# Optimization experiments

Measured on AMD Instinct MI355X. Metric: run time of the kernel, lower is better.

The kernel has to match this reference:

```python
import jax, jax.numpy as jnp
import numpy as np

R = 3.9
EPS = 0.3
BETA = 0.15
STEPS = 15
CLAMP = 1e-4


def setup_inputs() -> dict:
    key = jax.random.key(0)
    k1, k2 = jax.random.split(key)
    B, C, H, W = 64, 4, 512, 512
    drive = jax.random.uniform(k1, (B, C, H, W), dtype=jnp.float32)
    # frozen depthwise 3x3 kernel, normalized to sum 1 per channel (matches torch buffer init)
    K_raw = jnp.abs(jax.random.uniform(k2, (C, 1, 3, 3), dtype=jnp.float32))
    K = K_raw / jnp.sum(K_raw, axis=(-1, -2), keepdims=True)
    return {"drive": drive, "K": K}


def _depthwise_conv(x, K):
    # x: [B,C,H,W], K: [C,1,3,3] -> depthwise 3x3 conv, padding=1
    C = x.shape[1]
    return jax.lax.conv_general_dilated(
        x, K, window_strides=(1, 1), padding="SAME",
        dimension_numbers=("NCHW", "OIHW", "NCHW"),
        feature_group_count=C)


def reference(drive, K):
    grid = drive
    for _ in range(STEPS):
        mapped = R * grid * (1.0 - grid)          # logistic map
        local = _depthwise_conv(mapped, K)         # 3x3 depthwise coupling
        physics = (1.0 - EPS) * mapped + EPS * local
        grid = (1.0 - BETA) * physics + BETA * drive
    return jnp.clip(grid, CLAMP, 1.0 - CLAMP)
```

## Files before the change

kernel.cpp:

```cpp
#include <hip/hip_runtime.h>

#define IMG  512
#define TR   48
#define TC   112
#define RH   8
#define RLW  132
#define PR   66

__device__ __forceinline__ float mapf(float g) {
    float t = 3.9f * g;
    return t - t * g;
}

#define RD(P, M) do {                       \
    const float* _p = (P);                  \
    (M)[0] = _p[97 + pj];                   \
    (M)[1] = _p[pj];                        \
    (M)[2] = _p[33 + pj];                   \
    (M)[3] = _p[65 + pj];                   \
    (M)[4] = _p[98 + pj];                   \
    (M)[5] = _p[1 + pj];                    \
} while (0)

__global__ __launch_bounds__(512) void cml_round(
    const float* __restrict__ src,
    const float* __restrict__ drv,
    const float* __restrict__ Kw,
    float* __restrict__ dst,
    int steps, int do_clip)
{
    __shared__ float B[PR * RLW];

    const int tid = threadIdx.x;
    const int bid = blockIdx.x;
    const int bc  = bid / 55;
    const int tl  = bid % 55;
    const int gy0 = (tl / 5) * TR - RH;
    const int gx0 = (tl % 5) * TC - RH;
    const float* __restrict__ simg = src + (size_t)bc * (IMG*IMG);
    const float* __restrict__ dimg = drv + (size_t)bc * (IMG*IMG);
    float*       __restrict__ oimg = dst + (size_t)bc * (IMG*IMG);

    float kk[9];
    {
        const float c2 = 0.85f * 0.3f;
        const float* kp = Kw + (bc & 3) * 9;
#pragma unroll
        for (int q = 0; q < 9; q++) kk[q] = c2 * kp[q];
        kk[4] += 0.85f * 0.7f;
    }

    const int pj  = tid & 31;
    const int pi  = tid >> 5;
    const int y0  = pi * 4;
    const int gxb = gx0 + pj * 4;
    const float fxc = ((unsigned)gxb < IMG) ? 1.0f : 0.0f;

    float dvs[16];
#pragma unroll
    for (int rr = 0; rr < 4; rr++) {
        const int gy = gy0 + y0 + rr;
        float4 dv = make_float4(0.f, 0.f, 0.f, 0.f);
        if ((unsigned)gy < IMG && (unsigned)gxb < IMG)
            dv = *(const float4*)(dimg + gy*IMG + gxb);
        dvs[rr*4+0] = 0.15f * dv.x;
        dvs[rr*4+1] = 0.15f * dv.y;
        dvs[rr*4+2] = 0.15f * dv.z;
        dvs[rr*4+3] = 0.15f * dv.w;
    }

    for (int u = tid; u < PR * 32; u += 512) {
        const int r = u >> 5;
        const int p = u & 31;
        const int gy  = gy0 + r - 1;
        const int gxq = gx0 + p * 4;
        const bool rowok = (unsigned)gy < IMG;
        float4 v = make_float4(0.f, 0.f, 0.f, 0.f);
        if (rowok && (unsigned)gxq < IMG)
            v = *(const float4*)(simg + gy*IMG + gxq);
        float* row = B + r * RLW;
        row[p]      = mapf(v.x);
        row[33 + p] = mapf(v.y);
        row[65 + p] = mapf(v.z);
        row[98 + p] = mapf(v.w);
        if (p == 0) {
            float e = (rowok && (unsigned)(gx0 - 1) < IMG)
                    ? simg[gy*IMG + gx0 - 1] : 0.f;
            row[97] = mapf(e);
        }
        if (p == 31) {
            float e = (rowok && (unsigned)(gx0 + 128) < IMG)
                    ? simg[gy*IMG + gx0 + 128] : 0.f;
            row[32] = mapf(e);
        }
    }
    __syncthreads();

    float st[16];
#pragma unroll 1
    for (int step = 0; step < steps - 1; step++) {
        {
            float a[6], b6[6], c6[6];
            const float* p = B + y0 * RLW;
            RD(p, a);  p += RLW;
            RD(p, b6);
#pragma unroll
            for (int rr = 0; rr < 4; rr++) {
                p += RLW;
                RD(p, c6);
                const float ff = (((unsigned)(gy0 + y0 + rr) < IMG) ? 1.0f : 0.0f) * fxc;
#pragma unroll
                for (int k = 0; k < 4; k++) {
                    float s = dvs[rr*4+k];
                    s += kk[0]*a[k]  + kk[1]*a[k+1]  + kk[2]*a[k+2];
                    s += kk[3]*b6[k] + kk[4]*b6[k+1] + kk[5]*b6[k+2];
                    s += kk[6]*c6[k] + kk[7]*c6[k+1] + kk[8]*c6[k+2];
                    const float t = 3.9f * s;
                    st[rr*4+k] = (t - t*s) * ff;
                }
#pragma unroll
                for (int q = 0; q < 6; q++) { a[q] = b6[q]; b6[q] = c6[q]; }
            }
        }
        __syncthreads();
#pragma unroll
        for (int rr = 0; rr < 4; rr++) {
            float* w = B + (y0 + 1 + rr) * RLW;
            w[pj]      = st[rr*4+0];
            w[33 + pj] = st[rr*4+1];
            w[65 + pj] = st[rr*4+2];
            w[98 + pj] = st[rr*4+3];
        }
        __syncthreads();
    }

    {
        float a[6], b6[6], c6[6];
        const float* p = B + y0 * RLW;
        RD(p, a);  p += RLW;
        RD(p, b6);
#pragma unroll
        for (int rr = 0; rr < 4; rr++) {
            p += RLW;
            RD(p, c6);
#pragma unroll
            for (int k = 0; k < 4; k++) {
                float s = dvs[rr*4+k];
                s += kk[0]*a[k]  + kk[1]*a[k+1]  + kk[2]*a[k+2];
                s += kk[3]*b6[k] + kk[4]*b6[k+1] + kk[5]*b6[k+2];
                s += kk[6]*c6[k] + kk[7]*c6[k+1] + kk[8]*c6[k+2];
                st[rr*4+k] = s;
            }
#pragma unroll
            for (int q = 0; q < 6; q++) { a[q] = b6[q]; b6[q] = c6[q]; }
        }
    }
    if (pi >= 2 && pi <= 13 && pj >= 2 && pj <= 29) {
#pragma unroll
        for (int rr = 0; rr < 4; rr++) {
            const int gy = gy0 + y0 + rr;
            if (gy < IMG && gxb + 3 < IMG) {
                float4 v = make_float4(st[rr*4+0], st[rr*4+1],
                                       st[rr*4+2], st[rr*4+3]);
                if (do_clip) {
                    v.x = fminf(fmaxf(v.x, 1e-4f), 1.0f - 1e-4f);
                    v.y = fminf(fmaxf(v.y, 1e-4f), 1.0f - 1e-4f);
                    v.z = fminf(fmaxf(v.z, 1e-4f), 1.0f - 1e-4f);
                    v.w = fminf(fmaxf(v.w, 1e-4f), 1.0f - 1e-4f);
                }
                *(float4*)(oimg + gy*IMG + gxb) = v;
            }
        }
    }
}

#define TILE  128
#define OFF_Y 16
#define OFF_X 18
#define BUFY  160
#define BUFX  164
#define LW    172
#define NP    1014

__device__ __forceinline__ void read_row6(const float* __restrict__ p, int xw,
                                          float* m) {
    const float4 mid = *(const float4*)(p + xw + 4);
    m[0] = p[xw + 3];
    m[1] = mid.x; m[2] = mid.y; m[3] = mid.z; m[4] = mid.w;
    m[5] = p[xw + 8];
}

__global__ __launch_bounds__(1024, 4) void cml_fused(
    const float* __restrict__ drive,
    const float* __restrict__ Kw,
    float* __restrict__ out)
{
    __shared__ float lds[BUFY * LW];
    const int tid = threadIdx.x;
    const int bid = blockIdx.x;
    const int bc  = bid >> 4;
    const int tl  = bid & 15;
    const int gy0 = (tl >> 2) * TILE - OFF_Y;
    const int gx0 = (tl & 3)  * TILE - OFF_X;
    const float* __restrict__ img  = drive + (size_t)bc * (IMG*IMG);
    float*       __restrict__ oimg = out   + (size_t)bc * (IMG*IMG);
    float kk[9];
    {
        const float c2 = 0.85f * 0.3f;
        const float* kp = Kw + (bc & 3) * 9;
#pragma unroll
        for (int q = 0; q < 9; q++) kk[q] = c2 * kp[q];
        kk[4] += 0.85f * 0.7f;
    }
    const int t2 = tid < NP ? tid : NP - 1;
    const int pi = t2 / 39;
    const int pj = t2 - pi * 39;
    const int y0 = 2 + 6 * pi;
    const int xw = 4 * pj;
    float dvs[24], fx[4], fy[6];
#pragma unroll
    for (int k = 0; k < 4; k++)
        fx[k] = ((unsigned)(gx0 + xw + 4 + k) < IMG) ? 1.0f : 0.0f;
#pragma unroll
    for (int rr = 0; rr < 6; rr++) {
        const int gy = gy0 + y0 + rr;
        fy[rr] = ((unsigned)gy < IMG) ? 1.0f : 0.0f;
#pragma unroll
        for (int k = 0; k < 4; k++) {
            const int gx = gx0 + xw + 4 + k;
            dvs[rr*4+k] = (((unsigned)gy < IMG) && ((unsigned)gx < IMG))
                        ? 0.15f * img[gy*IMG + gx] : 0.0f;
        }
    }
    for (int u = tid; u < BUFY * (LW/2); u += 1024) {
        const int yy = u / (LW/2);
        const int xx = (u - yy * (LW/2)) * 2;
        const int gy = gy0 + yy;
        const int gxb = gx0 + xx;
        float2 v = make_float2(0.f, 0.f);
        if (xx < BUFX && (unsigned)gy < IMG && (unsigned)gxb < IMG)
            v = *(const float2*)(img + gy*IMG + gxb);
        v.x = mapf(v.x); v.y = mapf(v.y);
        *(float2*)(lds + yy*LW + xx) = v;
    }
    __syncthreads();
    float st[24];
#pragma unroll 1
    for (int step = 0; step < 14; step++) {
        {
            float a[6], b[6], c[6];
            const float* p = lds + (y0 - 1) * LW;
            read_row6(p, xw, a);  p += LW;
            read_row6(p, xw, b);
#pragma unroll
            for (int rr = 0; rr < 6; rr++) {
                p += LW;
                read_row6(p, xw, c);
                const float fyr = fy[rr];
#pragma unroll
                for (int k = 0; k < 4; k++) {
                    float s = dvs[rr*4+k];
                    s += kk[0]*a[k] + kk[1]*a[k+1] + kk[2]*a[k+2];
                    s += kk[3]*b[k] + kk[4]*b[k+1] + kk[5]*b[k+2];
                    s += kk[6]*c[k] + kk[7]*c[k+1] + kk[8]*c[k+2];
                    const float t = 3.9f * s;
                    st[rr*4+k] = (t - t*s) * fyr * fx[k];
                }
#pragma unroll
                for (int q = 0; q < 6; q++) { a[q] = b[q]; b[q] = c[q]; }
            }
        }
        __syncthreads();
        {
            float* w = lds + y0 * LW + xw + 4;
#pragma unroll
            for (int rr = 0; rr < 6; rr++) {
                *(float4*)w = make_float4(st[rr*4+0], st[rr*4+1],
                                          st[rr*4+2], st[rr*4+3]);
                w += LW;
            }
        }
        __syncthreads();
    }
    {
        float a[6], b[6], c[6];
        const float* p = lds + (y0 - 1) * LW;
        read_row6(p, xw, a);  p += LW;
        read_row6(p, xw, b);
#pragma unroll
        for (int rr = 0; rr < 6; rr++) {
            p += LW;
            read_row6(p, xw, c);
#pragma unroll
            for (int k = 0; k < 4; k++) {
                float s = dvs[rr*4+k];
                s += kk[0]*a[k] + kk[1]*a[k+1] + kk[2]*a[k+2];
                s += kk[3]*b[k] + kk[4]*b[k+1] + kk[5]*b[k+2];
                s += kk[6]*c[k] + kk[7]*c[k+1] + kk[8]*c[k+2];
                st[rr*4+k] = fminf(fmaxf(s, 1e-4f), 1.0f - 1e-4f);
            }
#pragma unroll
            for (int q = 0; q < 6; q++) { a[q] = b[q]; b[q] = c[q]; }
        }
    }
#pragma unroll
    for (int rr = 0; rr < 6; rr++) {
        const int r = y0 + rr;
        if (r >= OFF_Y && r < OFF_Y + TILE) {
#pragma unroll
            for (int h = 0; h < 2; h++) {
                const int col = xw + 4 + 2*h;
                if (col >= OFF_X && col + 1 < OFF_X + TILE) {
                    *(float2*)(oimg + (size_t)(gy0 + r) * IMG + (gx0 + col)) =
                        make_float2(st[rr*4 + 2*h], st[rr*4 + 2*h + 1]);
                }
            }
        }
    }
}

extern "C" void kernel_launch(void* const* d_in, const int* in_sizes, int n_in,
                              void* d_out, int out_size, void* d_ws, size_t ws_size,
                              hipStream_t stream)
{
    const float* drive = (const float*)d_in[0];
    const float* Kw    = (const float*)d_in[1];
    float* out         = (float*)d_out;
    const size_t need  = (size_t)256 * IMG * IMG * sizeof(float);

    if (ws_size >= need) {
        float* g8 = (float*)d_ws;
        cml_round<<<dim3(14080), dim3(512), 0, stream>>>(drive, drive, Kw, g8, 8, 0);
        cml_round<<<dim3(14080), dim3(512), 0, stream>>>(g8, drive, Kw, out, 7, 1);
    } else {
        cml_fused<<<dim3(4096), dim3(1024), 0, stream>>>(drive, Kw, out);
    }
}
```

Measured before the change: 831.9 us.

## Double-buffer LDS grid and keep each thread's own rows in registers

The single shared tile becomes two ping-pong buffers, so each step needs one barrier instead of two. Each thread now keeps its own 4x4 block of the state in registers across steps and reads only the halo (top and bottom rows, left and right edge columns) from LDS, which cuts LDS read traffic. The cost is twice the LDS per block, which can lower the number of resident blocks per CU. The border rows and columns of the second buffer are never initialised. That is only safe if the halo width covers every step of a round.

```diff
diff --git a/kernel.cpp b/kernel.cpp
--- a/kernel.cpp
+++ b/kernel.cpp
@@ -6,20 +6,18 @@
 #define RH   8
 #define RLW  132
 #define PR   66
+#define BUFSZ (PR * RLW)
 
 __device__ __forceinline__ float mapf(float g) {
     float t = 3.9f * g;
     return t - t * g;
 }
 
-#define RD(P, M) do {                       \
+#define RDROW(P, M) do {                    \
     const float* _p = (P);                  \
-    (M)[0] = _p[97 + pj];                   \
-    (M)[1] = _p[pj];                        \
-    (M)[2] = _p[33 + pj];                   \
-    (M)[3] = _p[65 + pj];                   \
-    (M)[4] = _p[98 + pj];                   \
-    (M)[5] = _p[1 + pj];                    \
+    (M)[0] = _p[97]; (M)[5] = _p[1];        \
+    (M)[1] = _p[0];  (M)[4] = _p[98];       \
+    (M)[2] = _p[33]; (M)[3] = _p[65];       \
 } while (0)
 
 __global__ __launch_bounds__(512) void cml_round(
@@ -29,7 +27,7 @@
     float* __restrict__ dst,
     int steps, int do_clip)
 {
-    __shared__ float B[PR * RLW];
+    __shared__ float Bd[2 * BUFSZ];
 
     const int tid = threadIdx.x;
     const int bid = blockIdx.x;
@@ -56,6 +54,11 @@
     const int gxb = gx0 + pj * 4;
     const float fxc = ((unsigned)gxb < IMG) ? 1.0f : 0.0f;
 
+    float ffr[4];
+#pragma unroll
+    for (int rr = 0; rr < 4; rr++)
+        ffr[rr] = (((unsigned)(gy0 + y0 + rr) < IMG) ? 1.0f : 0.0f) * fxc;
+
     float dvs[16];
 #pragma unroll
     for (int rr = 0; rr < 4; rr++) {
@@ -78,7 +81,7 @@
         float4 v = make_float4(0.f, 0.f, 0.f, 0.f);
         if (rowok && (unsigned)gxq < IMG)
             v = *(const float4*)(simg + gy*IMG + gxq);
-        float* row = B + r * RLW;
+        float* row = Bd + r * RLW;
         row[p]      = mapf(v.x);
         row[33 + p] = mapf(v.y);
         row[65 + p] = mapf(v.z);
@@ -97,62 +100,127 @@
     __syncthreads();
 
     float st[16];
+    {
+        const float* q1 = Bd + (y0 + 1) * RLW + pj;
+        const float* q3 = q1 + 2 * RLW;
+        st[0]  = q1[0];        st[4]  = q1[RLW];
+        st[1]  = q1[33];       st[5]  = q1[33 + RLW];
+        st[2]  = q1[65];       st[6]  = q1[65 + RLW];
+        st[3]  = q1[98];       st[7]  = q1[98 + RLW];
+        st[8]  = q3[0];        st[12] = q3[RLW];
+        st[9]  = q3[33];       st[13] = q3[33 + RLW];
+        st[10] = q3[65];       st[14] = q3[65 + RLW];
+        st[11] = q3[98];       st[15] = q3[98 + RLW];
+    }
+
+    float* cur = Bd;
+    float* nxt = Bd + BUFSZ;
+
 #pragma unroll 1
     for (int step = 0; step < steps - 1; step++) {
-        {
-            float a[6], b6[6], c6[6];
-            const float* p = B + y0 * RLW;
-            RD(p, a);  p += RLW;
-            RD(p, b6);
-#pragma unroll
-            for (int rr = 0; rr < 4; rr++) {
-                p += RLW;
-                RD(p, c6);
-                const float ff = (((unsigned)(gy0 + y0 + rr) < IMG) ? 1.0f : 0.0f) * fxc;
-#pragma unroll
-                for (int k = 0; k < 4; k++) {
-                    float s = dvs[rr*4+k];
-                    s += kk[0]*a[k]  + kk[1]*a[k+1]  + kk[2]*a[k+2];
-                    s += kk[3]*b6[k] + kk[4]*b6[k+1] + kk[5]*b6[k+2];
-                    s += kk[6]*c6[k] + kk[7]*c6[k+1] + kk[8]*c6[k+2];
-                    const float t = 3.9f * s;
-                    st[rr*4+k] = (t - t*s) * ff;
-                }
-#pragma unroll
-                for (int q = 0; q < 6; q++) { a[q] = b6[q]; b6[q] = c6[q]; }
-            }
-        }
-        __syncthreads();
+        const float* p0 = cur + y0 * RLW + pj;
+        const float* p5 = p0 + 5 * RLW;
+        const float* p1 = p0 + RLW;
+        const float* p3 = p0 + 3 * RLW;
+        float top[6], bot[6], lef[4], rig[4];
+        RDROW(p0, top);
+        RDROW(p5, bot);
+        lef[0] = p1[97];  lef[1] = p1[97 + RLW];
+        lef[2] = p3[97];  lef[3] = p3[97 + RLW];
+        rig[0] = p1[1];   rig[1] = p1[1 + RLW];
+        rig[2] = p3[1];   rig[3] = p3[1 + RLW];
+
+        float a[6], b[6], c[6];
+#pragma unroll
+        for (int q = 0; q < 6; q++) a[q] = top[q];
+        b[0] = lef[0]; b[1] = st[0]; b[2] = st[1];
+        b[3] = st[2];  b[4] = st[3]; b[5] = rig[0];
 #pragma unroll
         for (int rr = 0; rr < 4; rr++) {
-            float* w = B + (y0 + 1 + rr) * RLW;
-            w[pj]      = st[rr*4+0];
-            w[33 + pj] = st[rr*4+1];
-            w[65 + pj] = st[rr*4+2];
-            w[98 + pj] = st[rr*4+3];
-        }
-        __syncthreads();
-    }
-
-    {
-        float a[6], b6[6], c6[6];
-        const float* p = B + y0 * RLW;
-        RD(p, a);  p += RLW;
-        RD(p, b6);
-#pragma unroll
-        for (int rr = 0; rr < 4; rr++) {
-            p += RLW;
-            RD(p, c6);
+            if (rr < 3) {
+                c[0] = lef[rr+1];
+                c[1] = st[(rr+1)*4+0]; c[2] = st[(rr+1)*4+1];
+                c[3] = st[(rr+1)*4+2]; c[4] = st[(rr+1)*4+3];
+                c[5] = rig[rr+1];
+            } else {
+#pragma unroll
+                for (int q = 0; q < 6; q++) c[q] = bot[q];
+            }
+            const float ff = ffr[rr];
+            float ns[4];
 #pragma unroll
             for (int k = 0; k < 4; k++) {
                 float s = dvs[rr*4+k];
-                s += kk[0]*a[k]  + kk[1]*a[k+1]  + kk[2]*a[k+2];
-                s += kk[3]*b6[k] + kk[4]*b6[k+1] + kk[5]*b6[k+2];
-                s += kk[6]*c6[k] + kk[7]*c6[k+1] + kk[8]*c6[k+2];
-                st[rr*4+k] = s;
-            }
-#pragma unroll
-            for (int q = 0; q < 6; q++) { a[q] = b6[q]; b6[q] = c6[q]; }
+                s += kk[0]*a[k] + kk[1]*a[k+1] + kk[2]*a[k+2];
+                s += kk[3]*b[k] + kk[4]*b[k+1] + kk[5]*b[k+2];
+                s += kk[6]*c[k] + kk[7]*c[k+1] + kk[8]*c[k+2];
+                const float t = 3.9f * s;
+                ns[k] = (t - t*s) * ff;
+            }
+#pragma unroll
+            for (int q = 0; q < 6; q++) { a[q] = b[q]; b[q] = c[q]; }
+#pragma unroll
+            for (int k = 0; k < 4; k++) st[rr*4+k] = ns[k];
+        }
+
+        {
+            float* w1 = nxt + (y0 + 1) * RLW + pj;
+            float* w3 = w1 + 2 * RLW;
+            w1[0]  = st[0];   w1[RLW]      = st[4];
+            w1[33] = st[1];   w1[33 + RLW] = st[5];
+            w1[65] = st[2];   w1[65 + RLW] = st[6];
+            w1[98] = st[3];   w1[98 + RLW] = st[7];
+            w3[0]  = st[8];   w3[RLW]      = st[12];
+            w3[33] = st[9];   w3[33 + RLW] = st[13];
+            w3[65] = st[10];  w3[65 + RLW] = st[14];
+            w3[98] = st[11];  w3[98 + RLW] = st[15];
+        }
+        __syncthreads();
+        float* tmp = cur; cur = nxt; nxt = tmp;
+    }
+
+    {
+        const float* p0 = cur + y0 * RLW + pj;
+        const float* p5 = p0 + 5 * RLW;
+        const float* p1 = p0 + RLW;
+        const float* p3 = p0 + 3 * RLW;
+        float top[6], bot[6], lef[4], rig[4];
+        RDROW(p0, top);
+        RDROW(p5, bot);
+        lef[0] = p1[97];  lef[1] = p1[97 + RLW];
+        lef[2] = p3[97];  lef[3] = p3[97 + RLW];
+        rig[0] = p1[1];   rig[1] = p1[1 + RLW];
+        rig[2] = p3[1];   rig[3] = p3[1 + RLW];
+
+        float a[6], b[6], c[6];
+#pragma unroll
+        for (int q = 0; q < 6; q++) a[q] = top[q];
+        b[0] = lef[0]; b[1] = st[0]; b[2] = st[1];
+        b[3] = st[2];  b[4] = st[3]; b[5] = rig[0];
+#pragma unroll
+        for (int rr = 0; rr < 4; rr++) {
+            if (rr < 3) {
+                c[0] = lef[rr+1];
+                c[1] = st[(rr+1)*4+0]; c[2] = st[(rr+1)*4+1];
+                c[3] = st[(rr+1)*4+2]; c[4] = st[(rr+1)*4+3];
+                c[5] = rig[rr+1];
+            } else {
+#pragma unroll
+                for (int q = 0; q < 6; q++) c[q] = bot[q];
+            }
+            float ns[4];
+#pragma unroll
+            for (int k = 0; k < 4; k++) {
+                float s = dvs[rr*4+k];
+                s += kk[0]*a[k] + kk[1]*a[k+1] + kk[2]*a[k+2];
+                s += kk[3]*b[k] + kk[4]*b[k+1] + kk[5]*b[k+2];
+                s += kk[6]*c[k] + kk[7]*c[k+1] + kk[8]*c[k+2];
+                ns[k] = s;
+            }
+#pragma unroll
+            for (int q = 0; q < 6; q++) { a[q] = b[q]; b[q] = c[q]; }
+#pragma unroll
+            for (int k = 0; k < 4; k++) st[rr*4+k] = ns[k];
         }
     }
     if (pi >= 2 && pi <= 13 && pj >= 2 && pj <= 29) {
```

After: 838.1 us. About the same (+0.7%).
